# Kernel tuning notes

Measured on AMD Instinct MI355X. Metric: run time of the kernel, lower is better.

Reference implementation:

```python
import jax, jax.numpy as jnp
import numpy as np

N = 131072   # num_nodes
E = 262144   # events in the batch
D = 128      # memory_dim
R = 128      # raw_msg_dim
T = 32       # time_dim


def setup_inputs() -> dict:
    key = jax.random.key(0)
    ks = jax.random.split(key, 16)
    s = 0.05
    return {
        "memory": jax.random.normal(ks[0], (N, D), jnp.float32) * s,
        "raw_msg": jax.random.normal(ks[1], (E, R), jnp.float32) * s,
        "time_w": jax.random.normal(ks[2], (T,), jnp.float32) * s,
        "time_b": jax.random.normal(ks[3], (T,), jnp.float32) * s,
        "W_msg_s": jax.random.normal(ks[4], (D, 2 * D + R + T), jnp.float32) * s,
        "b_msg_s": jax.random.normal(ks[5], (D,), jnp.float32) * s,
        "W_msg_d": jax.random.normal(ks[6], (D, 2 * D + R + T), jnp.float32) * s,
        "b_msg_d": jax.random.normal(ks[7], (D,), jnp.float32) * s,
        "W_ih": jax.random.normal(ks[8], (3 * D, D), jnp.float32) * s,
        "W_hh": jax.random.normal(ks[9], (3 * D, D), jnp.float32) * s,
        "b_ih": jax.random.normal(ks[10], (3 * D,), jnp.float32) * s,
        "b_hh": jax.random.normal(ks[11], (3 * D,), jnp.float32) * s,
        "src": jax.random.randint(ks[12], (E,), 0, N, jnp.int32),
        "dst": jax.random.randint(ks[13], (E,), 0, N, jnp.int32),
        "t": jax.random.randint(ks[14], (E,), 0, 100000, jnp.int32),
        "last_update": jax.random.randint(ks[15], (N,), 0, 50000, jnp.int32),
    }


def _time_enc(t_rel, time_w, time_b):
    # TimeEncoder: cos(Linear(t)) ; t_rel: [E] float -> [E, T]
    return jnp.cos(t_rel[:, None] * time_w[None, :] + time_b[None, :])


def _message(mem_a, mem_b, raw_msg, t_enc, W, b):
    # message MLP on concat(mem_src, mem_dst, raw_msg, t_enc)
    x = jnp.concatenate([mem_a, mem_b, raw_msg, t_enc], axis=-1)  # [E, 2D+R+T]
    return jax.nn.relu(x @ W.T + b)


def _forward(memory, raw_msg, time_w, time_b, W_msg_s, b_msg_s, W_msg_d, b_msg_d,
             W_ih, W_hh, b_ih, b_hh, src, dst, t, last_update):
    tf = t.astype(jnp.float32)
    lu = last_update.astype(jnp.float32)
    mem_s = memory[src]  # gather [E, D]
    mem_d = memory[dst]

    # source-side messages (stored under key src): t_rel = t - last_update[src]
    t_enc_s = _time_enc(tf - lu[src], time_w, time_b)
    msg_s = _message(mem_s, mem_d, raw_msg, t_enc_s, W_msg_s, b_msg_s)
    # dest-side messages (stored under key dst, src/dst swapped)
    t_enc_d = _time_enc(tf - lu[dst], time_w, time_b)
    msg_d = _message(mem_d, mem_s, raw_msg, t_enc_d, W_msg_d, b_msg_d)

    # scatter mean-aggregate messages onto their owner node
    seg = jnp.concatenate([src, dst], axis=0)          # [2E]
    vals = jnp.concatenate([msg_s, msg_d], axis=0)     # [2E, D]
    sums = jax.ops.segment_sum(vals, seg, num_segments=N)
    cnt = jax.ops.segment_sum(jnp.ones((2 * E,), jnp.float32), seg, num_segments=N)
    aggr = sums / jnp.maximum(cnt, 1.0)[:, None]       # [N, D]

    # GRUCell(aggr, memory)
    gi = aggr @ W_ih.T + b_ih
    gh = memory @ W_hh.T + b_hh
    i_r, i_z, i_n = jnp.split(gi, 3, axis=-1)
    h_r, h_z, h_n = jnp.split(gh, 3, axis=-1)
    r = jax.nn.sigmoid(i_r + h_r)
    z = jax.nn.sigmoid(i_z + h_z)
    n = jnp.tanh(i_n + r * h_n)
    new_memory = (1.0 - z) * n + z * memory

    # scatter-max timestamps (pyg scatter reduce='max' fills empty slots with 0)
    tt = jnp.concatenate([t, t], axis=0)
    seg_max = jax.ops.segment_max(tt, seg, num_segments=N)
    new_last_update = jnp.where(cnt > 0, seg_max, jnp.zeros((), jnp.int32))
    return new_memory, new_last_update


def reference(memory, raw_msg, time_w, time_b, W_msg_s, b_msg_s, W_msg_d, b_msg_d,
              W_ih, W_hh, b_ih, b_hh, src, dst, t, last_update):
    return _forward(memory, raw_msg, time_w, time_b, W_msg_s, b_msg_s, W_msg_d,
                    b_msg_d, W_ih, W_hh, b_ih, b_hh, src, dst, t, last_update)
```

## Files before the change

### kernel.cpp

```cpp
#include <hip/hip_runtime.h>
#include <cstdint>
#include <cstddef>

#define NN 131072
#define EE 262144

typedef __attribute__((ext_vector_type(8))) short bf16x8;
typedef __attribute__((ext_vector_type(4))) float f32x4;

__device__ __forceinline__ unsigned short f2bf(float f) {
    unsigned int u = __builtin_bit_cast(unsigned int, f);
    u += 0x7FFFu + ((u >> 16) & 1u);
    return (unsigned short)(u >> 16);
}
__device__ __forceinline__ float bf2f(unsigned short s) {
    unsigned int u = ((unsigned int)s) << 16;
    return __builtin_bit_cast(float, u);
}
__device__ __forceinline__ float sigmoidf_(float x) { return 1.0f / (1.0f + __expf(-x)); }
__device__ __forceinline__ float tanhf_(float x) {
    float ax = fabsf(x);
    float e = __expf(-2.0f * ax);
    return copysignf((1.0f - e) / (1.0f + e), x);
}
__device__ __forceinline__ bf16x8 pack8(const float* f) {
    bf16x8 o;
#pragma unroll
    for (int i = 0; i < 8; ++i) o[i] = (short)f2bf(f[i]);
    return o;
}

__device__ __forceinline__ float wmsg_val(int n, int k, const float* Ws, const float* Wd) {
    if (n < 128) {
        return (k < 416) ? Ws[n * 416 + k] : 0.0f;
    } else {
        int m = n - 128;
        if (k < 128)       return Wd[m * 416 + 128 + k];
        else if (k < 256)  return Wd[m * 416 + (k - 128)];
        else if (k < 384)  return Wd[m * 416 + k];
        else if (k < 416)  return 0.0f;
        else               return Wd[m * 416 + 384 + (k - 416)];
    }
}
__device__ __forceinline__ float wgru_val(int j, int k, const float* Wih, const float* Whh) {
    if (j < 256)      return (k < 128) ? Wih[j * 128 + k] : Whh[j * 128 + (k - 128)];
    else if (j < 384) return (k < 128) ? Wih[j * 128 + k] : 0.0f;
    else              return (k < 128) ? 0.0f : Whh[(j - 128) * 128 + (k - 128)];
}

__global__ void k_prep_msgfrag(const float* __restrict__ Ws, const float* __restrict__ Wd,
                               const float* __restrict__ bs, const float* __restrict__ bd,
                               unsigned short* __restrict__ Wmf, float* __restrict__ bm) {
    int b = blockIdx.x;
    int c = b >> 4, nt = b & 15;
    int lane = threadIdx.x;
    int col0 = lane & 15, q = lane >> 4;
    int n = nt * 16 + col0;
    float f[8];
#pragma unroll
    for (int j = 0; j < 8; ++j) f[j] = wmsg_val(n, c * 32 + q * 8 + j, Ws, Wd);
    ((bf16x8*)Wmf)[(size_t)b * 64 + lane] = pack8(f);
    if (b == 0)
        for (int i = lane; i < 256; i += 64) bm[i] = (i < 128) ? bs[i] : bd[i - 128];
}

__global__ void k_prep_grufrag(const float* __restrict__ Wih, const float* __restrict__ Whh,
                               const float* __restrict__ bih, const float* __restrict__ bhh,
                               unsigned short* __restrict__ Wgf, float* __restrict__ bg) {
    int b = blockIdx.x;
    int c = b >> 5, nt = b & 31;
    int lane = threadIdx.x;
    int col0 = lane & 15, q = lane >> 4;
    int j0 = nt * 16 + col0;
    float f[8];
#pragma unroll
    for (int j = 0; j < 8; ++j) f[j] = wgru_val(j0, c * 32 + q * 8 + j, Wih, Whh);
    ((bf16x8*)Wgf)[(size_t)b * 64 + lane] = pack8(f);
    if (b == 0)
        for (int i = lane; i < 512; i += 64)
            bg[i] = (i < 256) ? (bih[i] + bhh[i]) : ((i < 384) ? bih[i] : bhh[i - 128]);
}

__global__ void k_memconv(const float* __restrict__ in, unsigned short* __restrict__ outp) {
    int gid = blockIdx.x * 256 + threadIdx.x;
    const float4 v = ((const float4*)in)[gid];
    ushort4 o;
    o.x = f2bf(v.x); o.y = f2bf(v.y); o.z = f2bf(v.z); o.w = f2bf(v.w);
    *(ushort4*)(outp + (size_t)gid * 4) = o;
}

__global__ void k_pre(const int* __restrict__ t, const int* __restrict__ src,
                      const int* __restrict__ dst, const int* __restrict__ lu,
                      float* __restrict__ trel_s, float* __restrict__ trel_d,
                      int* cnt, int* lu_tmp) {
    int e = blockIdx.x * 256 + threadIdx.x;
    int s = src[e], d = dst[e], tv = t[e];
    trel_s[e] = (float)(tv - lu[s]);
    trel_d[e] = (float)(tv - lu[d]);
    atomicAdd(&cnt[s], 1);
    atomicAdd(&cnt[d], 1);
    atomicMax(&lu_tmp[s], tv);
    atomicMax(&lu_tmp[d], tv);
}

__global__ void k_scan1(const int* __restrict__ cnt, int* __restrict__ bsum) {
    __shared__ int red[256];
    int tid = threadIdx.x;
    red[tid] = cnt[blockIdx.x * 256 + tid];
    __syncthreads();
    for (int s = 128; s > 0; s >>= 1) {
        if (tid < s) red[tid] += red[tid + s];
        __syncthreads();
    }
    if (tid == 0) bsum[blockIdx.x] = red[0];
}
__global__ void k_scan2(const int* __restrict__ bsum, int* __restrict__ boff) {
    __shared__ int sb[512];
    int tid = threadIdx.x;
    int v = bsum[tid];
    sb[tid] = v;
    __syncthreads();
    for (int d = 1; d < 512; d <<= 1) {
        int u = (tid >= d) ? sb[tid - d] : 0;
        __syncthreads();
        sb[tid] += u;
        __syncthreads();
    }
    boff[tid] = sb[tid] - v;
}
__global__ void k_scan3(const int* __restrict__ cnt, const int* __restrict__ boff,
                        int* __restrict__ off, int* __restrict__ cursor) {
    __shared__ int sb[256];
    int tid = threadIdx.x;
    int i = blockIdx.x * 256 + tid;
    int v = cnt[i];
    sb[tid] = v;
    __syncthreads();
    for (int d = 1; d < 256; d <<= 1) {
        int u = (tid >= d) ? sb[tid - d] : 0;
        __syncthreads();
        sb[tid] += u;
        __syncthreads();
    }
    int o = boff[blockIdx.x] + sb[tid] - v;
    off[i] = o;
    cursor[i] = o;
}
__global__ void k_fill(const int* __restrict__ src, const int* __restrict__ dst,
                       int* cursor, int* __restrict__ pos2) {
    int e2 = blockIdx.x * 256 + threadIdx.x;
    int node = (e2 < EE) ? src[e2] : dst[e2 - EE];
    pos2[e2] = atomicAdd(&cursor[node], 1);
}

__launch_bounds__(256, 2)
__global__ void k_msg(const unsigned short* __restrict__ memb,
                      const float* __restrict__ raw,
                      const float* __restrict__ trel_s,
                      const float* __restrict__ trel_d,
                      const unsigned short* __restrict__ Wmf,
                      const float* __restrict__ bm,
                      const int* __restrict__ src, const int* __restrict__ dst,
                      const int* __restrict__ pos2,
                      const float* __restrict__ tw, const float* __restrict__ tb,
                      unsigned short* __restrict__ msg) {
    __shared__ int s_idx[128], d_idx[128], s_pos[128], d_pos[128];
    __shared__ float s_tw[32], s_tb[32];
    __shared__ __align__(16) unsigned short As[2][128 * 40];

    const int tid = threadIdx.x;
    const int e0 = blockIdx.x * 128;
    if (tid < 128) { s_idx[tid] = src[e0 + tid]; s_pos[tid] = pos2[e0 + tid]; }
    else { d_idx[tid - 128] = dst[e0 + tid - 128]; d_pos[tid - 128] = pos2[EE + e0 + tid - 128]; }
    if (tid < 32)       s_tw[tid] = tw[tid];
    else if (tid < 64)  s_tb[tid - 32] = tb[tid - 32];
    __syncthreads();

    const int lane = tid & 63, w = tid >> 6;
    const int col0 = lane & 15, q = lane >> 4;

    auto stage = [&](int cc) {
        unsigned short* A = As[cc & 1];
        if (cc < 8) {
#pragma unroll
            for (int i = 0; i < 2; ++i) {
                int lin = tid + 256 * i;
                int row = lin >> 2, seg = lin & 3;
                int node = (cc < 4) ? s_idx[row] : d_idx[row];
                bf16x8 v = *(const bf16x8*)(memb + (size_t)node * 128 + (cc & 3) * 32 + seg * 8);
                *(bf16x8*)&A[row * 40 + seg * 8] = v;
            }
        } else if (cc < 12) {
#pragma unroll
            for (int i = 0; i < 4; ++i) {
                int lin = tid + 256 * i;
                int row = lin >> 3, seg = lin & 7;
                const float4 v = *(const float4*)(raw + (size_t)(e0 + row) * 128 + (cc - 8) * 32 + seg * 4);
                ushort4 o;
                o.x = f2bf(v.x); o.y = f2bf(v.y); o.z = f2bf(v.z); o.w = f2bf(v.w);
                *(ushort4*)&A[row * 40 + seg * 4] = o;
            }
        } else {
            int row = tid >> 1, half = tid & 1;
            float tr = (cc == 12) ? trel_s[e0 + row] : trel_d[e0 + row];
            float f[16];
#pragma unroll
            for (int j2 = 0; j2 < 16; ++j2) {
                int jj = half * 16 + j2;
                f[j2] = __cosf(tr * s_tw[jj] + s_tb[jj]);
            }
            *(bf16x8*)&A[row * 40 + half * 16] = pack8(&f[0]);
            *(bf16x8*)&A[row * 40 + half * 16 + 8] = pack8(&f[8]);
        }
    };

    f32x4 acc[8][4];
#pragma unroll
    for (int a = 0; a < 8; ++a)
#pragma unroll
        for (int b = 0; b < 4; ++b)
#pragma unroll
            for (int i = 0; i < 4; ++i) acc[a][b][i] = 0.0f;

    stage(0);
    __syncthreads();

    for (int c = 0; c < 14; ++c) {
        bf16x8 bfr[4];
        const bf16x8* Wc = (const bf16x8*)Wmf + (size_t)c * 16 * 64;
#pragma unroll
        for (int nl = 0; nl < 4; ++nl)
            bfr[nl] = Wc[(w * 4 + nl) * 64 + lane];
        const unsigned short* A = As[c & 1];
        bf16x8 afr[8];
#pragma unroll
        for (int mt = 0; mt < 8; ++mt)
            afr[mt] = *(const bf16x8*)&A[(mt * 16 + col0) * 40 + q * 8];
        if (c < 13) stage(c + 1);
#pragma unroll
        for (int mt = 0; mt < 8; ++mt)
#pragma unroll
            for (int nl = 0; nl < 4; ++nl)
                acc[mt][nl] = __builtin_amdgcn_mfma_f32_16x16x32_bf16(afr[mt], bfr[nl], acc[mt][nl], 0, 0, 0);
        __syncthreads();
    }

#pragma unroll
    for (int nl = 0; nl < 4; ++nl) {
        int j = (w * 4 + nl) * 16 + col0;
        float bv = bm[j];
        int feat = j & 127;
        bool is_s = (j < 128);
#pragma unroll
        for (int mt = 0; mt < 8; ++mt) {
#pragma unroll
            for (int r = 0; r < 4; ++r) {
                int ev = mt * 16 + q * 4 + r;
                float v = fmaxf(acc[mt][nl][r] + bv, 0.0f);
                int pos = is_s ? s_pos[ev] : d_pos[ev];
                msg[(size_t)pos * 128 + feat] = f2bf(v);
            }
        }
    }
}

__launch_bounds__(256, 3)
__global__ void k_gru(const unsigned short* __restrict__ msg,
                      const int* __restrict__ off, const int* __restrict__ cnt,
                      const float* __restrict__ memory,
                      const unsigned short* __restrict__ Wgf,
                      const float* __restrict__ bg,
                      float* __restrict__ out) {
    __shared__ __align__(16) unsigned short Xs[32 * 264];

    const int tid = threadIdx.x;
    const int n0 = blockIdx.x * 32;

    {
        int g = tid >> 3, sub = tid & 7;
        int node = n0 + g;
        int beg = off[node], cn = cnt[node];
        float a[16];
#pragma unroll
        for (int i = 0; i < 16; ++i) a[i] = 0.0f;
        for (int m = 0; m < cn; ++m) {
            const bf16x8* p = (const bf16x8*)(msg + (size_t)(beg + m) * 128 + sub * 16);
            bf16x8 v0 = p[0], v1 = p[1];
#pragma unroll
            for (int k = 0; k < 8; ++k) {
                a[k]     += bf2f((unsigned short)v0[k]);
                a[8 + k] += bf2f((unsigned short)v1[k]);
            }
        }
        float inv = 1.0f / (float)(cn > 1 ? cn : 1);
#pragma unroll
        for (int i = 0; i < 16; ++i) a[i] *= inv;
        *(bf16x8*)&Xs[g * 264 + sub * 16] = pack8(&a[0]);
        *(bf16x8*)&Xs[g * 264 + sub * 16 + 8] = pack8(&a[8]);
        float f[16];
        const float4* mp = (const float4*)(memory + (size_t)node * 128 + sub * 16);
#pragma unroll
        for (int s = 0; s < 4; ++s) {
            float4 v = mp[s];
            f[s * 4 + 0] = v.x; f[s * 4 + 1] = v.y; f[s * 4 + 2] = v.z; f[s * 4 + 3] = v.w;
        }
        *(bf16x8*)&Xs[g * 264 + 128 + sub * 16] = pack8(&f[0]);
        *(bf16x8*)&Xs[g * 264 + 128 + sub * 16 + 8] = pack8(&f[8]);
    }
    __syncthreads();

    const int lane = tid & 63, w = tid >> 6;
    const int col0 = lane & 15, q = lane >> 4;

    f32x4 acc[2][4][2];
#pragma unroll
    for (int a = 0; a < 2; ++a)
#pragma unroll
        for (int g = 0; g < 4; ++g)
#pragma unroll
            for (int f = 0; f < 2; ++f)
#pragma unroll
                for (int i = 0; i < 4; ++i) acc[a][g][f][i] = 0.0f;

#pragma unroll
    for (int c = 0; c < 8; ++c) {
        bf16x8 bfr[4][2];
        const bf16x8* Wc = (const bf16x8*)Wgf + (size_t)c * 32 * 64;
#pragma unroll
        for (int g = 0; g < 4; ++g)
#pragma unroll
            for (int fh = 0; fh < 2; ++fh)
                bfr[g][fh] = Wc[(8 * g + 2 * w + fh) * 64 + lane];
        bf16x8 afr[2];
#pragma unroll
        for (int mt = 0; mt < 2; ++mt)
            afr[mt] = *(const bf16x8*)&Xs[(mt * 16 + col0) * 264 + c * 32 + q * 8];
#pragma unroll
        for (int mt = 0; mt < 2; ++mt)
#pragma unroll
            for (int g = 0; g < 4; ++g)
#pragma unroll
                for (int fh = 0; fh < 2; ++fh)
                    acc[mt][g][fh] = __builtin_amdgcn_mfma_f32_16x16x32_bf16(afr[mt], bfr[g][fh], acc[mt][g][fh], 0, 0, 0);
    }

#pragma unroll
    for (int fh = 0; fh < 2; ++fh) {
        int feat = w * 32 + fh * 16 + col0;
        float b_r = bg[feat], b_z = bg[128 + feat], b_in = bg[256 + feat], b_hn = bg[384 + feat];
#pragma unroll
        for (int mt = 0; mt < 2; ++mt) {
#pragma unroll
            for (int r = 0; r < 4; ++r) {
                int node = n0 + mt * 16 + q * 4 + r;
                float rr = sigmoidf_(acc[mt][0][fh][r] + b_r);
                float zz = sigmoidf_(acc[mt][1][fh][r] + b_z);
                float nn = tanhf_((acc[mt][2][fh][r] + b_in) + rr * (acc[mt][3][fh][r] + b_hn));
                float h = memory[(size_t)node * 128 + feat];
                out[(size_t)node * 128 + feat] = (1.0f - zz) * nn + zz * h;
            }
        }
    }
}

__global__ void k_lu(const int* __restrict__ lu_tmp, float* __restrict__ outp) {
    int i = blockIdx.x * 256 + threadIdx.x;
    outp[i] = (float)lu_tmp[i];
}

extern "C" void kernel_launch(void* const* d_in, const int* in_sizes, int n_in,
                              void* d_out, int out_size, void* d_ws, size_t ws_size,
                              hipStream_t stream) {
    const float* memory = (const float*)d_in[0];
    const float* raw    = (const float*)d_in[1];
    const float* tw     = (const float*)d_in[2];
    const float* tb     = (const float*)d_in[3];
    const float* Wms    = (const float*)d_in[4];
    const float* bms    = (const float*)d_in[5];
    const float* Wmd    = (const float*)d_in[6];
    const float* bmd    = (const float*)d_in[7];
    const float* Wih    = (const float*)d_in[8];
    const float* Whh    = (const float*)d_in[9];
    const float* bih    = (const float*)d_in[10];
    const float* bhh    = (const float*)d_in[11];
    const int* src = (const int*)d_in[12];
    const int* dst = (const int*)d_in[13];
    const int* t   = (const int*)d_in[14];
    const int* lu  = (const int*)d_in[15];

    char* ws = (char*)d_ws;
    size_t ob = 0;
    unsigned short* memb = (unsigned short*)(ws + ob); ob += (size_t)NN * 128 * 2;
    unsigned short* msg  = (unsigned short*)(ws + ob); ob += (size_t)2 * EE * 128 * 2;
    float* trel_s        = (float*)(ws + ob);          ob += (size_t)EE * 4;
    float* trel_d        = (float*)(ws + ob);          ob += (size_t)EE * 4;
    int* cnt             = (int*)(ws + ob);            ob += (size_t)NN * 4;
    int* off             = (int*)(ws + ob);            ob += (size_t)NN * 4;
    int* cursor          = (int*)(ws + ob);            ob += (size_t)NN * 4;
    int* lu_tmp          = (int*)(ws + ob);            ob += (size_t)NN * 4;
    int* pos2            = (int*)(ws + ob);            ob += (size_t)2 * EE * 4;
    int* bsum            = (int*)(ws + ob);            ob += 512 * 4;
    int* boff            = (int*)(ws + ob);            ob += 512 * 4;
    unsigned short* Wmf  = (unsigned short*)(ws + ob); ob += (size_t)14 * 16 * 64 * 8 * 2;
    float* bm            = (float*)(ws + ob);          ob += 256 * 4;
    unsigned short* Wgf  = (unsigned short*)(ws + ob); ob += (size_t)8 * 32 * 64 * 8 * 2;
    float* bg            = (float*)(ws + ob);          ob += 512 * 4;

    float* out = (float*)d_out;

    hipMemsetAsync(cnt, 0, (size_t)NN * 4, stream);
    hipMemsetAsync(lu_tmp, 0, (size_t)NN * 4, stream);

    k_prep_msgfrag<<<14 * 16, 64, 0, stream>>>(Wms, Wmd, bms, bmd, Wmf, bm);
    k_prep_grufrag<<<8 * 32, 64, 0, stream>>>(Wih, Whh, bih, bhh, Wgf, bg);
    k_memconv<<<(NN * 128 / 4) / 256, 256, 0, stream>>>(memory, memb);
    k_pre<<<EE / 256, 256, 0, stream>>>(t, src, dst, lu, trel_s, trel_d, cnt, lu_tmp);
    k_scan1<<<512, 256, 0, stream>>>(cnt, bsum);
    k_scan2<<<1, 512, 0, stream>>>(bsum, boff);
    k_scan3<<<512, 256, 0, stream>>>(cnt, boff, off, cursor);
    k_fill<<<2 * EE / 256, 256, 0, stream>>>(src, dst, cursor, pos2);
    k_msg<<<EE / 128, 256, 0, stream>>>(memb, raw, trel_s, trel_d, Wmf, bm, src, dst, pos2, tw, tb, msg);
    k_gru<<<NN / 32, 256, 0, stream>>>(msg, off, cnt, memory, Wgf, bg, out);
    k_lu<<<NN / 256, 256, 0, stream>>>(lu_tmp, out + (size_t)NN * 128);
}
```

Measured before the change: 579.0 us.

## Precompute time encoding, register-prefetch operands, and coalesce message stores via LDS

Time encodings are now computed by a separate kernel into bf16 buffers placed in the output memory as scratch, and read by k_msg like the other operands. k_msg splits staging into issue (global loads into registers) and commit (LDS writes), and prefetches the next weight fragments, so global latency overlaps the MFMA work. The epilogue writes results through shared memory so each CSR row is stored as full 256-byte segments instead of scattered 2-byte writes. In exchange there is an extra kernel launch and extra global traffic for the tenc buffers, higher register pressure, and the output buffer is reused as scratch before k_gru overwrites it.

New measurement: 588.9 us. Within noise of the previous version (+1.7%).

```diff
diff --git a/kernel.cpp b/kernel.cpp
--- a/kernel.cpp
+++ b/kernel.cpp
@@ -89,14 +89,25 @@
     *(ushort4*)(outp + (size_t)gid * 4) = o;
 }
 
-__global__ void k_pre(const int* __restrict__ t, const int* __restrict__ src,
-                      const int* __restrict__ dst, const int* __restrict__ lu,
-                      float* __restrict__ trel_s, float* __restrict__ trel_d,
-                      int* cnt, int* lu_tmp) {
+__global__ void k_tenc(const int* __restrict__ t, const int* __restrict__ src,
+                       const int* __restrict__ dst, const int* __restrict__ lu,
+                       const float* __restrict__ tw, const float* __restrict__ tb,
+                       unsigned short* __restrict__ tenc_s, unsigned short* __restrict__ tenc_d) {
+    int gid = blockIdx.x * 256 + threadIdx.x;
+    int e = gid >> 6;
+    int j = gid & 63;
+    int jj = j & 31;
+    int node = (j < 32) ? src[e] : dst[e];
+    float tr = (float)(t[e] - lu[node]);
+    unsigned short v = f2bf(__cosf(tr * tw[jj] + tb[jj]));
+    if (j < 32) tenc_s[(size_t)e * 32 + jj] = v;
+    else        tenc_d[(size_t)e * 32 + jj] = v;
+}
+
+__global__ void k_pre(const int* __restrict__ src, const int* __restrict__ dst,
+                      const int* __restrict__ t, int* cnt, int* lu_tmp) {
     int e = blockIdx.x * 256 + threadIdx.x;
     int s = src[e], d = dst[e], tv = t[e];
-    trel_s[e] = (float)(tv - lu[s]);
-    trel_d[e] = (float)(tv - lu[d]);
     atomicAdd(&cnt[s], 1);
     atomicAdd(&cnt[d], 1);
     atomicMax(&lu_tmp[s], tv);
@@ -156,61 +167,68 @@
 __launch_bounds__(256, 2)
 __global__ void k_msg(const unsigned short* __restrict__ memb,
                       const float* __restrict__ raw,
-                      const float* __restrict__ trel_s,
-                      const float* __restrict__ trel_d,
+                      const unsigned short* __restrict__ tenc_s,
+                      const unsigned short* __restrict__ tenc_d,
                       const unsigned short* __restrict__ Wmf,
                       const float* __restrict__ bm,
                       const int* __restrict__ src, const int* __restrict__ dst,
                       const int* __restrict__ pos2,
-                      const float* __restrict__ tw, const float* __restrict__ tb,
                       unsigned short* __restrict__ msg) {
     __shared__ int s_idx[128], d_idx[128], s_pos[128], d_pos[128];
-    __shared__ float s_tw[32], s_tb[32];
-    __shared__ __align__(16) unsigned short As[2][128 * 40];
+    __shared__ __align__(16) unsigned short As[2][5120];
 
     const int tid = threadIdx.x;
     const int e0 = blockIdx.x * 128;
     if (tid < 128) { s_idx[tid] = src[e0 + tid]; s_pos[tid] = pos2[e0 + tid]; }
     else { d_idx[tid - 128] = dst[e0 + tid - 128]; d_pos[tid - 128] = pos2[EE + e0 + tid - 128]; }
-    if (tid < 32)       s_tw[tid] = tw[tid];
-    else if (tid < 64)  s_tb[tid - 32] = tb[tid - 32];
     __syncthreads();
 
     const int lane = tid & 63, w = tid >> 6;
     const int col0 = lane & 15, q = lane >> 4;
 
-    auto stage = [&](int cc) {
+    bf16x8 sreg[2];
+    float4 rreg[4];
+
+    auto issue = [&](int cc) {
+        if (cc < 8) {
+#pragma unroll
+            for (int i = 0; i < 2; ++i) {
+                int lin = tid + 256 * i, row = lin >> 2, seg = lin & 3;
+                int node = (cc < 4) ? s_idx[row] : d_idx[row];
+                sreg[i] = *(const bf16x8*)(memb + (size_t)node * 128 + (cc & 3) * 32 + seg * 8);
+            }
+        } else if (cc < 12) {
+#pragma unroll
+            for (int i = 0; i < 4; ++i) {
+                int lin = tid + 256 * i, row = lin >> 3, seg = lin & 7;
+                rreg[i] = *(const float4*)(raw + (size_t)(e0 + row) * 128 + (cc - 8) * 32 + seg * 4);
+            }
+        } else {
+            const unsigned short* tp = (cc == 12) ? tenc_s : tenc_d;
+#pragma unroll
+            for (int i = 0; i < 2; ++i) {
+                int lin = tid + 256 * i, row = lin >> 2, seg = lin & 3;
+                sreg[i] = *(const bf16x8*)(tp + (size_t)(e0 + row) * 32 + seg * 8);
+            }
+        }
+    };
+    auto commit = [&](int cc) {
         unsigned short* A = As[cc & 1];
-        if (cc < 8) {
+        if (cc < 8 || cc >= 12) {
 #pragma unroll
             for (int i = 0; i < 2; ++i) {
-                int lin = tid + 256 * i;
-                int row = lin >> 2, seg = lin & 3;
-                int node = (cc < 4) ? s_idx[row] : d_idx[row];
-                bf16x8 v = *(const bf16x8*)(memb + (size_t)node * 128 + (cc & 3) * 32 + seg * 8);
-                *(bf16x8*)&A[row * 40 + seg * 8] = v;
-            }
-        } else if (cc < 12) {
+                int lin = tid + 256 * i, row = lin >> 2, seg = lin & 3;
+                *(bf16x8*)&A[row * 40 + seg * 8] = sreg[i];
+            }
+        } else {
 #pragma unroll
             for (int i = 0; i < 4; ++i) {
-                int lin = tid + 256 * i;
-                int row = lin >> 3, seg = lin & 7;
-                const float4 v = *(const float4*)(raw + (size_t)(e0 + row) * 128 + (cc - 8) * 32 + seg * 4);
+                int lin = tid + 256 * i, row = lin >> 3, seg = lin & 7;
                 ushort4 o;
-                o.x = f2bf(v.x); o.y = f2bf(v.y); o.z = f2bf(v.z); o.w = f2bf(v.w);
+                o.x = f2bf(rreg[i].x); o.y = f2bf(rreg[i].y);
+                o.z = f2bf(rreg[i].z); o.w = f2bf(rreg[i].w);
                 *(ushort4*)&A[row * 40 + seg * 4] = o;
             }
-        } else {
-            int row = tid >> 1, half = tid & 1;
-            float tr = (cc == 12) ? trel_s[e0 + row] : trel_d[e0 + row];
-            float f[16];
-#pragma unroll
-            for (int j2 = 0; j2 < 16; ++j2) {
-                int jj = half * 16 + j2;
-                f[j2] = __cosf(tr * s_tw[jj] + s_tb[jj]);
-            }
-            *(bf16x8*)&A[row * 40 + half * 16] = pack8(&f[0]);
-            *(bf16x8*)&A[row * 40 + half * 16 + 8] = pack8(&f[8]);
         }
     };
 
@@ -222,45 +240,73 @@
 #pragma unroll
             for (int i = 0; i < 4; ++i) acc[a][b][i] = 0.0f;
 
-    stage(0);
+    const bf16x8* WmfV = (const bf16x8*)Wmf;
+    bf16x8 bcur[4], bnxt[4];
+#pragma unroll
+    for (int nl = 0; nl < 4; ++nl)
+        bcur[nl] = WmfV[(size_t)(0 * 16 + w * 4 + nl) * 64 + lane];
+    issue(0);
+    commit(0);
     __syncthreads();
 
     for (int c = 0; c < 14; ++c) {
-        bf16x8 bfr[4];
-        const bf16x8* Wc = (const bf16x8*)Wmf + (size_t)c * 16 * 64;
-#pragma unroll
-        for (int nl = 0; nl < 4; ++nl)
-            bfr[nl] = Wc[(w * 4 + nl) * 64 + lane];
+        if (c < 13) {
+#pragma unroll
+            for (int nl = 0; nl < 4; ++nl)
+                bnxt[nl] = WmfV[(size_t)((c + 1) * 16 + w * 4 + nl) * 64 + lane];
+            issue(c + 1);
+        }
         const unsigned short* A = As[c & 1];
         bf16x8 afr[8];
 #pragma unroll
         for (int mt = 0; mt < 8; ++mt)
             afr[mt] = *(const bf16x8*)&A[(mt * 16 + col0) * 40 + q * 8];
-        if (c < 13) stage(c + 1);
 #pragma unroll
         for (int mt = 0; mt < 8; ++mt)
 #pragma unroll
             for (int nl = 0; nl < 4; ++nl)
-                acc[mt][nl] = __builtin_amdgcn_mfma_f32_16x16x32_bf16(afr[mt], bfr[nl], acc[mt][nl], 0, 0, 0);
-        __syncthreads();
-    }
-
-#pragma unroll
-    for (int nl = 0; nl < 4; ++nl) {
-        int j = (w * 4 + nl) * 16 + col0;
-        float bv = bm[j];
-        int feat = j & 127;
-        bool is_s = (j < 128);
-#pragma unroll
-        for (int mt = 0; mt < 8; ++mt) {
-#pragma unroll
-            for (int r = 0; r < 4; ++r) {
-                int ev = mt * 16 + q * 4 + r;
-                float v = fmaxf(acc[mt][nl][r] + bv, 0.0f);
-                int pos = is_s ? s_pos[ev] : d_pos[ev];
-                msg[(size_t)pos * 128 + feat] = f2bf(v);
-            }
-        }
+                acc[mt][nl] = __builtin_amdgcn_mfma_f32_16x16x32_bf16(afr[mt], bcur[nl], acc[mt][nl], 0, 0, 0);
+        if (c < 13) commit(c + 1);
+        __syncthreads();
+#pragma unroll
+        for (int nl = 0; nl < 4; ++nl) bcur[nl] = bnxt[nl];
+    }
+
+    float bv[4];
+#pragma unroll
+    for (int nl = 0; nl < 4; ++nl) bv[nl] = bm[(w * 4 + nl) * 16 + col0];
+    unsigned short* C = &As[0][0];
+#pragma unroll
+    for (int p = 0; p < 4; ++p) {
+        __syncthreads();
+        const bool s_side = (p < 2);
+        const int evb = (p & 1) * 64;
+        if ((w < 2) == s_side) {
+#pragma unroll
+            for (int nl = 0; nl < 4; ++nl) {
+                int jj = ((w & 1) * 4 + nl) * 16 + col0;
+#pragma unroll
+                for (int mt2 = 0; mt2 < 4; ++mt2) {
+                    int mt = (p & 1) * 4 + mt2;
+#pragma unroll
+                    for (int r = 0; r < 4; ++r) {
+                        int lr = mt2 * 16 + q * 4 + r;
+                        float v = fmaxf(acc[mt][nl][r] + bv[nl], 0.0f);
+                        C[lr * 136 + jj] = f2bf(v);
+                    }
+                }
+            }
+        }
+        __syncthreads();
+        int lr = tid >> 2, seg = tid & 3;
+        int ev = evb + lr;
+        int pos = s_side ? s_pos[ev] : d_pos[ev];
+        const bf16x8* cp = (const bf16x8*)&C[lr * 136 + seg * 32];
+        bf16x8* gp = (bf16x8*)(msg + (size_t)pos * 128 + seg * 32);
+        gp[0] = cp[0];
+        gp[1] = cp[1];
+        gp[2] = cp[2];
+        gp[3] = cp[3];
     }
 }
 
@@ -392,8 +438,6 @@
     size_t ob = 0;
     unsigned short* memb = (unsigned short*)(ws + ob); ob += (size_t)NN * 128 * 2;
     unsigned short* msg  = (unsigned short*)(ws + ob); ob += (size_t)2 * EE * 128 * 2;
-    float* trel_s        = (float*)(ws + ob);          ob += (size_t)EE * 4;
-    float* trel_d        = (float*)(ws + ob);          ob += (size_t)EE * 4;
     int* cnt             = (int*)(ws + ob);            ob += (size_t)NN * 4;
     int* off             = (int*)(ws + ob);            ob += (size_t)NN * 4;
     int* cursor          = (int*)(ws + ob);            ob += (size_t)NN * 4;
@@ -407,6 +451,8 @@
     float* bg            = (float*)(ws + ob);          ob += 512 * 4;
 
     float* out = (float*)d_out;
+    unsigned short* tenc_s = (unsigned short*)d_out;
+    unsigned short* tenc_d = tenc_s + (size_t)EE * 32;
 
     hipMemsetAsync(cnt, 0, (size_t)NN * 4, stream);
     hipMemsetAsync(lu_tmp, 0, (size_t)NN * 4, stream);
@@ -414,12 +460,13 @@
     k_prep_msgfrag<<<14 * 16, 64, 0, stream>>>(Wms, Wmd, bms, bmd, Wmf, bm);
     k_prep_grufrag<<<8 * 32, 64, 0, stream>>>(Wih, Whh, bih, bhh, Wgf, bg);
     k_memconv<<<(NN * 128 / 4) / 256, 256, 0, stream>>>(memory, memb);
-    k_pre<<<EE / 256, 256, 0, stream>>>(t, src, dst, lu, trel_s, trel_d, cnt, lu_tmp);
+    k_tenc<<<(EE * 64) / 256, 256, 0, stream>>>(t, src, dst, lu, tw, tb, tenc_s, tenc_d);
+    k_pre<<<EE / 256, 256, 0, stream>>>(src, dst, t, cnt, lu_tmp);
     k_scan1<<<512, 256, 0, stream>>>(cnt, bsum);
     k_scan2<<<1, 512, 0, stream>>>(bsum, boff);
     k_scan3<<<512, 256, 0, stream>>>(cnt, boff, off, cursor);
     k_fill<<<2 * EE / 256, 256, 0, stream>>>(src, dst, cursor, pos2);
-    k_msg<<<EE / 128, 256, 0, stream>>>(memb, raw, trel_s, trel_d, Wmf, bm, src, dst, pos2, tw, tb, msg);
+    k_msg<<<EE / 128, 256, 0, stream>>>(memb, raw, tenc_s, tenc_d, Wmf, bm, src, dst, pos2, msg);
     k_gru<<<NN / 32, 256, 0, stream>>>(msg, off, cnt, memory, Wgf, bg, out);
     k_lu<<<NN / 256, 256, 0, stream>>>(lu_tmp, out + (size_t)NN * 128);
 }
```
